# Performance work log

Hardware: AMD Instinct MI355X
Metric: run time of the kernel (lower is better)

The kernel has to match this reference:

```python
import jax, jax.numpy as jnp
import numpy as np

B, C, H, W = 2, 128, 64, 64
D_STATE, D_CONV, EXPAND = 16, 4, 2
D_INNER = EXPAND * C
DT_RANK = (C + 15) // 16  # ceil(d_model/16) = 8


def layernorm(x, w, b):
    # WithBias_LayerNorm over last (channel) dim, unbiased=False variance
    mu = jnp.mean(x, axis=-1, keepdims=True)
    var = jnp.mean((x - mu) ** 2, axis=-1, keepdims=True)
    return (x - mu) / jnp.sqrt(var + 1e-5) * w + b


def causal_conv1d_silu(x, w, b):
    # x: (b, d, l); w: (d, k) depthwise; causal pad k-1 on left, then SiLU
    k = w.shape[1]
    out = jax.lax.conv_general_dilated(
        x, w[:, None, :], window_strides=(1,), padding=[(k - 1, 0)],
        dimension_numbers=('NCH', 'OIH', 'NCH'), feature_group_count=w.shape[0])
    return jax.nn.silu(out + b[:, None])


def selective_scan(dA, dBu, Cm):
    # dA, dBu: (b, d, l, n); Cm: (b, n, l) -> y: (b, d, l)
    dA_t = jnp.moveaxis(dA, 2, 0)    # (l, b, d, n)
    dBu_t = jnp.moveaxis(dBu, 2, 0)  # (l, b, d, n)
    C_t = jnp.moveaxis(Cm, 2, 0)     # (l, b, n)

    def step(h, inp):
        a, bu, c = inp
        h = a * h + bu
        y = jnp.einsum('bdn,bn->bd', h, c)
        return h, y

    h0 = jnp.zeros(dA.shape[:2] + (dA.shape[3],), dA.dtype)
    _, ys = jax.lax.scan(step, h0, (dA_t, dBu_t, C_t))
    return jnp.moveaxis(ys, 0, 2)  # (b, d, l)


def mamba_branch(x3, W_in, W_z, conv_w, conv_b, W_x, W_dt, b_dt, A, D, W_out):
    # x3: (b, l, d_model) normalized input
    x = jnp.einsum('bld,ed->bel', x3, W_in)  # (b, d_inner, l)
    z = jnp.einsum('bld,ed->bel', x3, W_z)
    x = causal_conv1d_silu(x, conv_w, conv_b)
    xdbl = jnp.einsum('bdl,ed->bel', x, W_x)  # (b, dt_rank+2n, l)
    dt_low = xdbl[:, :DT_RANK]
    Bm = xdbl[:, DT_RANK:DT_RANK + D_STATE]
    Cm = xdbl[:, DT_RANK + D_STATE:]
    delta = jax.nn.softplus(jnp.einsum('brl,dr->bdl', dt_low, W_dt) + b_dt[:, None])
    dA = jnp.exp(delta[:, :, :, None] * A[None, :, None, :])           # (b,d,l,n)
    dBu = jnp.einsum('bdl,bnl->bdln', delta * x, Bm)                    # (b,d,l,n)
    y = selective_scan(dA, dBu, Cm)
    y = y + D[:, None] * x
    y = y * jax.nn.silu(z)
    return jnp.einsum('bdl,od->blo', y, W_out)  # (b, l, d_model)


def setup_inputs() -> dict:
    key = jax.random.key(0)
    ks = jax.random.split(key, 24)
    rn = lambda k, shp, s: jax.random.normal(k, shp, dtype=jnp.float32) * s
    inp = {}
    inp['pan'] = rn(ks[0], (B, C, H, W), 1.0)
    inp['ms'] = rn(ks[1], (B, C, H, W), 1.0)
    inp['norm_w_pan'] = jnp.ones((C,), jnp.float32)
    inp['norm_b_pan'] = jnp.zeros((C,), jnp.float32)
    inp['norm_w_ms'] = jnp.ones((C,), jnp.float32)
    inp['norm_b_ms'] = jnp.zeros((C,), jnp.float32)
    inp['W_in_pan'] = rn(ks[2], (D_INNER, C), C ** -0.5)
    inp['W_in_ms'] = rn(ks[3], (D_INNER, C), C ** -0.5)
    inp['W_z_pan'] = rn(ks[4], (D_INNER, C), C ** -0.5)
    inp['W_z_ms'] = rn(ks[5], (D_INNER, C), C ** -0.5)
    inp['conv_w_pan'] = rn(ks[6], (D_INNER, D_CONV), D_CONV ** -0.5)
    inp['conv_b_pan'] = rn(ks[7], (D_INNER,), 0.02)
    inp['conv_w_ms'] = rn(ks[8], (D_INNER, D_CONV), D_CONV ** -0.5)
    inp['conv_b_ms'] = rn(ks[9], (D_INNER,), 0.02)
    inp['W_x_pan'] = rn(ks[10], (DT_RANK + 2 * D_STATE, D_INNER), D_INNER ** -0.5)
    inp['W_x_ms'] = rn(ks[11], (DT_RANK + 2 * D_STATE, D_INNER), D_INNER ** -0.5)
    dt_std = DT_RANK ** -0.5
    inp['W_dt_pan'] = jax.random.uniform(ks[12], (D_INNER, DT_RANK), jnp.float32, -dt_std, dt_std)
    inp['W_dt_ms'] = jax.random.uniform(ks[13], (D_INNER, DT_RANK), jnp.float32, -dt_std, dt_std)
    # dt bias init: inverse-softplus of dt ~ logU[1e-3, 1e-1]
    u = np.asarray(jax.random.uniform(ks[14], (D_INNER,)))
    dt = np.exp(u * (np.log(0.1) - np.log(0.001)) + np.log(0.001)).clip(min=1e-4)
    inv_dt = dt + np.log(-np.expm1(-dt))
    inp['b_dt_pan'] = jnp.asarray(inv_dt, jnp.float32)
    inp['b_dt_ms'] = jnp.asarray(inv_dt, jnp.float32)
    inp['A_log'] = jnp.log(jnp.broadcast_to(jnp.arange(1, D_STATE + 1, dtype=jnp.float32), (D_INNER, D_STATE)))
    inp['D_pan'] = jnp.ones((D_INNER,), jnp.float32)
    inp['D_ms'] = jnp.ones((D_INNER,), jnp.float32)
    inp['W_out_pan'] = rn(ks[15], (C, D_INNER), D_INNER ** -0.5)
    inp['W_out_ms'] = rn(ks[16], (C, D_INNER), D_INNER ** -0.5)
    return inp


def reference(pan, ms, norm_w_pan, norm_b_pan, norm_w_ms, norm_b_ms,
              W_in_pan, W_in_ms, W_z_pan, W_z_ms,
              conv_w_pan, conv_b_pan, conv_w_ms, conv_b_ms,
              W_x_pan, W_x_ms, W_dt_pan, W_dt_ms, b_dt_pan, b_dt_ms,
              A_log, D_pan, D_ms, W_out_pan, W_out_ms):
    b, c, h, w = pan.shape
    A = -jnp.exp(A_log)
    pan3 = layernorm(pan.reshape(b, c, h * w).transpose(0, 2, 1), norm_w_pan, norm_b_pan)
    ms3 = layernorm(ms.reshape(b, c, h * w).transpose(0, 2, 1), norm_w_ms, norm_b_ms)
    out_pan = mamba_branch(pan3, W_in_pan, W_z_pan, conv_w_pan, conv_b_pan,
                           W_x_pan, W_dt_pan, b_dt_pan, A, D_pan, W_out_pan)
    out_ms = mamba_branch(ms3, W_in_ms, W_z_ms, conv_w_ms, conv_b_ms,
                          W_x_ms, W_dt_ms, b_dt_ms, A, D_ms, W_out_ms)
    out_pan = out_pan.transpose(0, 2, 1).reshape(b, c, h, w)
    out_ms = out_ms.transpose(0, 2, 1).reshape(b, c, h, w)
    return (out_pan, out_ms)
```

## Files before the change

### kernel.cpp

```cpp
#include <hip/hip_runtime.h>
#include <hip/hip_bf16.h>

constexpr int BB = 2;
constexpr int CC = 128;
constexpr int LL = 4096;
constexpr int DI = 256;
constexpr int DS = 16;
constexpr int DR = 8;
constexpr int DX = 40;
constexpr int NZ = 2 * BB;
constexpr int CH = 8;
constexpr int NCH = LL / CH;
constexpr int SEG = 32;

typedef short bf16x8 __attribute__((ext_vector_type(8)));
typedef float f32x4 __attribute__((ext_vector_type(4)));
typedef float f32x2 __attribute__((ext_vector_type(2)));

__device__ __forceinline__ unsigned short f2bf(float x) {
    __hip_bfloat16 h = __float2bfloat16(x);
    return *(unsigned short*)&h;
}
__device__ __forceinline__ float bflo(unsigned u) { return __uint_as_float(u << 16); }
__device__ __forceinline__ float bfhi(unsigned u) { return __uint_as_float(u & 0xffff0000u); }
__device__ __forceinline__ float bfu(unsigned short u) { return __uint_as_float((unsigned)u << 16); }
__device__ __forceinline__ float fast_rcp(float x) { return __builtin_amdgcn_rcpf(x); }
__device__ __forceinline__ float siluf(float x) { return x * fast_rcp(1.f + __expf(-x)); }
__device__ __forceinline__ float softplusf(float x) {
    const float z = exp2f(x * 1.44269504f);
    return (x > 20.f) ? x : 0.69314718f * log2f(1.f + z);
}
__device__ __forceinline__ unsigned pk2(float lo, float hi) {
    return (unsigned)f2bf(lo) | ((unsigned)f2bf(hi) << 16);
}
__device__ __forceinline__ bf16x8 cvt8(const float4 a, const float4 b) {
    bf16x8 r;
    r[0] = (short)f2bf(a.x); r[1] = (short)f2bf(a.y);
    r[2] = (short)f2bf(a.z); r[3] = (short)f2bf(a.w);
    r[4] = (short)f2bf(b.x); r[5] = (short)f2bf(b.y);
    r[6] = (short)f2bf(b.z); r[7] = (short)f2bf(b.w);
    return r;
}

__global__ __launch_bounds__(256) void gemm_inz_mfma(
    const float* __restrict__ pan, const float* __restrict__ ms,
    const float* __restrict__ wpan, const float* __restrict__ bpan,
    const float* __restrict__ wms, const float* __restrict__ bms,
    const float* __restrict__ Winp, const float* __restrict__ Winm,
    const float* __restrict__ Wzp, const float* __restrict__ Wzm,
    unsigned short* __restrict__ xpre16, unsigned short* __restrict__ zb16)
{
    const int zi = blockIdx.z;
    const int my = blockIdx.y;
    const bool br = (zi >= BB);
    const float* WIf = br ? Winm : Winp;
    const float* WZf = br ? Wzm : Wzp;
    const float* inp = br ? ms : pan;
    const float* wln = br ? wms : wpan;
    const float* bln = br ? bms : bpan;
    const int mbase = my * 64;
    const int n0 = blockIdx.x * 64;
    const int t = threadIdx.x;
    const int w = t >> 6, ln = t & 63;
    const int nf = ln & 15, qb = ln >> 4;
    const int kp = t >> 4, n4 = (t & 15) * 4;

    bf16x8 afragI[4], afragZ[4];
    const int mrow = mbase + w * 16 + nf;
    #pragma unroll
    for (int c = 0; c < 4; c++) {
        const float* pi = WIf + (size_t)mrow * CC + c * 32 + qb * 8;
        const float* pz = WZf + (size_t)mrow * CC + c * 32 + qb * 8;
        afragI[c] = cvt8(*(const float4*)pi, *(const float4*)(pi + 4));
        afragZ[c] = cvt8(*(const float4*)pz, *(const float4*)(pz + 4));
    }

    const float* xbase = inp + (size_t)(zi & 1) * CC * LL + n0 + n4;
    float xv[8][4];
    float wrow[8], brow[8];
    float sm[4] = {}, sq[4] = {};
    #pragma unroll
    for (int j = 0; j < 8; j++) {
        const int r = (j >> 1) * 32 + 2 * kp + (j & 1);
        const float4 v = *(const float4*)(xbase + (size_t)r * LL);
        xv[j][0] = v.x; xv[j][1] = v.y; xv[j][2] = v.z; xv[j][3] = v.w;
        wrow[j] = wln[r]; brow[j] = bln[r];
        sm[0] += v.x; sm[1] += v.y; sm[2] += v.z; sm[3] += v.w;
        sq[0] += v.x * v.x; sq[1] += v.y * v.y; sq[2] += v.z * v.z; sq[3] += v.w * v.w;
    }
    __shared__ float redS[16][64];
    __shared__ float redQ[16][64];
    #pragma unroll
    for (int j = 0; j < 4; j++) { redS[kp][n4 + j] = sm[j]; redQ[kp][n4 + j] = sq[j]; }
    __syncthreads();
    float mu[4], rs[4];
    #pragma unroll
    for (int j = 0; j < 4; j++) { sm[j] = 0.f; sq[j] = 0.f; }
    #pragma unroll
    for (int k = 0; k < 16; k++)
        #pragma unroll
        for (int j = 0; j < 4; j++) { sm[j] += redS[k][n4 + j]; sq[j] += redQ[k][n4 + j]; }
    #pragma unroll
    for (int j = 0; j < 4; j++) {
        mu[j] = sm[j] * (1.f / CC);
        rs[j] = rsqrtf(sq[j] * (1.f / CC) - mu[j] * mu[j] + 1e-5f);
    }
    unsigned pk[4][4];
    #pragma unroll
    for (int kc = 0; kc < 4; kc++)
        #pragma unroll
        for (int j = 0; j < 4; j++) {
            const float lo = (xv[kc * 2 + 0][j] - mu[j]) * rs[j] * wrow[kc * 2 + 0] + brow[kc * 2 + 0];
            const float hi = (xv[kc * 2 + 1][j] - mu[j]) * rs[j] * wrow[kc * 2 + 1] + brow[kc * 2 + 1];
            pk[kc][j] = pk2(lo, hi);
        }

    __shared__ unsigned short Bs[64][40];
    unsigned* Bw = (unsigned*)Bs;
    f32x4 accI[4] = {}, accZ[4] = {};
    #pragma unroll
    for (int kc = 0; kc < 4; kc++) {
        if (kc) __syncthreads();
        Bw[(n4 + 0) * 20 + kp] = pk[kc][0];
        Bw[(n4 + 1) * 20 + kp] = pk[kc][1];
        Bw[(n4 + 2) * 20 + kp] = pk[kc][2];
        Bw[(n4 + 3) * 20 + kp] = pk[kc][3];
        __syncthreads();
        #pragma unroll
        for (int ns = 0; ns < 4; ns++) {
            const bf16x8 bf = *(const bf16x8*)(&Bs[ns * 16 + nf][qb * 8]);
            accI[ns] = __builtin_amdgcn_mfma_f32_16x16x32_bf16(afragI[kc], bf, accI[ns], 0, 0, 0);
            accZ[ns] = __builtin_amdgcn_mfma_f32_16x16x32_bf16(afragZ[kc], bf, accZ[ns], 0, 0, 0);
        }
    }
    #pragma unroll
    for (int ns = 0; ns < 4; ns++)
        #pragma unroll
        for (int r = 0; r < 4; r++) {
            const int m = mbase + w * 16 + qb * 4 + r;
            xpre16[((size_t)zi * DI + m) * LL + n0 + ns * 16 + nf] = f2bf(accI[ns][r]);
            zb16  [((size_t)zi * DI + m) * LL + n0 + ns * 16 + nf] = f2bf(siluf(accZ[ns][r]));
        }
}

__global__ __launch_bounds__(256) void gemm_x_mfma(
    const float* __restrict__ Wxp, const float* __restrict__ Wxm,
    const unsigned short* __restrict__ xpre16,
    const float* __restrict__ cw0, const float* __restrict__ cb0,
    const float* __restrict__ cw1, const float* __restrict__ cb1,
    unsigned short* __restrict__ xc, unsigned short* __restrict__ xdbl16)
{
    const int zi = blockIdx.z;
    const float* Wf = (zi >= BB) ? Wxm : Wxp;
    const float* cw = (zi >= BB) ? cw1 : cw0;
    const float* cb = (zi >= BB) ? cb1 : cb0;
    const unsigned short* Xb = xpre16 + (size_t)zi * DI * LL;
    unsigned short* xcb = xc + (size_t)zi * DI * LL;
    const int n0 = blockIdx.x * 64;
    const int t = threadIdx.x;
    const int w = t >> 6, ln = t & 63;
    const int nf = ln & 15, qb = ln >> 4;
    bf16x8 zfrag;
    #pragma unroll
    for (int j = 0; j < 8; j++) zfrag[j] = 0;
    bf16x8 afrag[8];
    const int mrow = w * 16 + nf;
    #pragma unroll
    for (int c = 0; c < 8; c++) {
        if (mrow < DX) {
            const float* p = Wf + (size_t)mrow * DI + c * 32 + qb * 8;
            afrag[c] = cvt8(*(const float4*)p, *(const float4*)(p + 4));
        } else afrag[c] = zfrag;
    }
    __shared__ unsigned short Bs[64][40];
    unsigned* Bw = (unsigned*)Bs;
    f32x4 acc[4] = {};
    const int kp = t >> 4, n4 = (t & 15) * 4;
    const bool edge = (n0 + n4 == 0);
    ushort4 cur0, cur1, prv0, prv1;
    {
        const unsigned short* xp0 = Xb + (size_t)(2 * kp) * LL + n0 + n4;
        const unsigned short* xp1 = Xb + (size_t)(2 * kp + 1) * LL + n0 + n4;
        cur0 = *(const ushort4*)xp0; cur1 = *(const ushort4*)xp1;
        if (!edge) { prv0 = *(const ushort4*)(xp0 - 4); prv1 = *(const ushort4*)(xp1 - 4); }
        else { prv0 = ushort4{0,0,0,0}; prv1 = ushort4{0,0,0,0}; }
    }
    #pragma unroll
    for (int kc = 0; kc < 8; kc++) {
        ushort4 o[2];
        #pragma unroll
        for (int rr = 0; rr < 2; rr++) {
            const int e = kc * 32 + 2 * kp + rr;
            const ushort4 cur = rr ? cur1 : cur0;
            const ushort4 prv = rr ? prv1 : prv0;
            const float xm3 = bfu(prv.y), xm2 = bfu(prv.z), xm1 = bfu(prv.w);
            const float c0 = bfu(cur.x), c1 = bfu(cur.y);
            const float c2 = bfu(cur.z), c3 = bfu(cur.w);
            const float w0 = cw[e * 4 + 0], w1 = cw[e * 4 + 1];
            const float w2 = cw[e * 4 + 2], w3 = cw[e * 4 + 3];
            const float bias = cb[e];
            o[rr].x = f2bf(siluf(w0 * xm3 + w1 * xm2 + w2 * xm1 + w3 * c0 + bias));
            o[rr].y = f2bf(siluf(w0 * xm2 + w1 * xm1 + w2 * c0 + w3 * c1 + bias));
            o[rr].z = f2bf(siluf(w0 * xm1 + w1 * c0 + w2 * c1 + w3 * c2 + bias));
            o[rr].w = f2bf(siluf(w0 * c0 + w1 * c1 + w2 * c2 + w3 * c3 + bias));
        }
        *(ushort4*)(xcb + (size_t)(kc * 32 + 2 * kp) * LL + n0 + n4) = o[0];
        *(ushort4*)(xcb + (size_t)(kc * 32 + 2 * kp + 1) * LL + n0 + n4) = o[1];
        if (kc) __syncthreads();
        Bw[(n4 + 0) * 20 + kp] = (unsigned)(unsigned short)o[0].x | ((unsigned)(unsigned short)o[1].x << 16);
        Bw[(n4 + 1) * 20 + kp] = (unsigned)(unsigned short)o[0].y | ((unsigned)(unsigned short)o[1].y << 16);
        Bw[(n4 + 2) * 20 + kp] = (unsigned)(unsigned short)o[0].z | ((unsigned)(unsigned short)o[1].z << 16);
        Bw[(n4 + 3) * 20 + kp] = (unsigned)(unsigned short)o[0].w | ((unsigned)(unsigned short)o[1].w << 16);
        __syncthreads();
        if (kc < 7) {
            const unsigned short* xp0 = Xb + (size_t)((kc + 1) * 32 + 2 * kp) * LL + n0 + n4;
            const unsigned short* xp1 = Xb + (size_t)((kc + 1) * 32 + 2 * kp + 1) * LL + n0 + n4;
            cur0 = *(const ushort4*)xp0; cur1 = *(const ushort4*)xp1;
            if (!edge) { prv0 = *(const ushort4*)(xp0 - 4); prv1 = *(const ushort4*)(xp1 - 4); }
        }
        #pragma unroll
        for (int ns = 0; ns < 4; ns++) {
            const bf16x8 bf = *(const bf16x8*)(&Bs[ns * 16 + nf][qb * 8]);
            acc[ns] = __builtin_amdgcn_mfma_f32_16x16x32_bf16(afrag[kc], bf, acc[ns], 0, 0, 0);
        }
    }
    #pragma unroll
    for (int ns = 0; ns < 4; ns++)
        #pragma unroll
        for (int r = 0; r < 4; r++) {
            const int m = w * 16 + qb * 4 + r;
            if (m < DX)
                xdbl16[((size_t)zi * DX + m) * LL + n0 + ns * 16 + nf] = f2bf(acc[ns][r]);
        }
}

__global__ __launch_bounds__(256) void gemm_out_mfma(
    const float* __restrict__ Woutp, const float* __restrict__ Woutm,
    const unsigned short* __restrict__ yb, float* __restrict__ outg)
{
    const int zi = blockIdx.z;
    const float* Wf = (zi >= BB) ? Woutm : Woutp;
    const int mbase = blockIdx.y * 64;
    const unsigned short* Xb = yb + (size_t)zi * DI * LL;
    const int n0 = blockIdx.x * 64;
    const int t = threadIdx.x;
    const int w = t >> 6, ln = t & 63;
    const int nf = ln & 15, qb = ln >> 4;
    bf16x8 afrag[8];
    const int mrow = mbase + w * 16 + nf;
    #pragma unroll
    for (int c = 0; c < 8; c++) {
        const float* p = Wf + (size_t)mrow * DI + c * 32 + qb * 8;
        afrag[c] = cvt8(*(const float4*)p, *(const float4*)(p + 4));
    }
    __shared__ unsigned short Bs[64][40];
    unsigned* Bw = (unsigned*)Bs;
    f32x4 acc[4] = {};
    const int kp = t >> 4, n4 = (t & 15) * 4;
    ushort4 a0 = *(const ushort4*)(Xb + (size_t)(2 * kp) * LL + n0 + n4);
    ushort4 a1 = *(const ushort4*)(Xb + (size_t)(2 * kp + 1) * LL + n0 + n4);
    #pragma unroll
    for (int kc = 0; kc < 8; kc++) {
        if (kc) __syncthreads();
        Bw[(n4 + 0) * 20 + kp] = (unsigned)a0.x | ((unsigned)a1.x << 16);
        Bw[(n4 + 1) * 20 + kp] = (unsigned)a0.y | ((unsigned)a1.y << 16);
        Bw[(n4 + 2) * 20 + kp] = (unsigned)a0.z | ((unsigned)a1.z << 16);
        Bw[(n4 + 3) * 20 + kp] = (unsigned)a0.w | ((unsigned)a1.w << 16);
        __syncthreads();
        if (kc < 7) {
            a0 = *(const ushort4*)(Xb + (size_t)((kc + 1) * 32 + 2 * kp) * LL + n0 + n4);
            a1 = *(const ushort4*)(Xb + (size_t)((kc + 1) * 32 + 2 * kp + 1) * LL + n0 + n4);
        }
        #pragma unroll
        for (int ns = 0; ns < 4; ns++) {
            const bf16x8 bf = *(const bf16x8*)(&Bs[ns * 16 + nf][qb * 8]);
            acc[ns] = __builtin_amdgcn_mfma_f32_16x16x32_bf16(afrag[kc], bf, acc[ns], 0, 0, 0);
        }
    }
    #pragma unroll
    for (int ns = 0; ns < 4; ns++)
        #pragma unroll
        for (int r = 0; r < 4; r++) {
            const int m = mbase + w * 16 + qb * 4 + r;
            outg[((size_t)zi * CC + m) * LL + n0 + ns * 16 + nf] = acc[ns][r];
        }
}

__global__ __launch_bounds__(512, 8) void scan_fused(
    const unsigned short* __restrict__ xc, const unsigned short* __restrict__ xdbl16,
    const float* __restrict__ A_log,
    const float* __restrict__ Wdt0, const float* __restrict__ Wdt1,
    const float* __restrict__ bdt0, const float* __restrict__ bdt1,
    const float* __restrict__ D0, const float* __restrict__ D1,
    const unsigned short* __restrict__ zb16, unsigned short* __restrict__ yb)
{
    const int blk = blockIdx.x;
    const int zi = blk >> 8;
    const int d  = blk & (DI - 1);
    const int t = threadIdx.x;
    const int l0 = t * CH;
    __shared__ float Ssh[DS * (NCH + 1)];
    __shared__ float sdl_sh[NCH];
    __shared__ float Pseg[DS * (SEG + 1)];
    __shared__ float Sseg[DS * (SEG + 1)];
    const unsigned short* xdb = xdbl16 + (size_t)zi * DX * LL;
    const float* Wdt = (zi >= BB) ? Wdt1 : Wdt0;
    const float* bdt = (zi >= BB) ? bdt1 : bdt0;
    const float dbias = bdt[d];
    float rx[CH];
    {
        const uint4 xv4 = *(const uint4*)(xc + (size_t)blk * LL + l0);
        rx[0] = bflo(xv4.x); rx[1] = bfhi(xv4.x);
        rx[2] = bflo(xv4.y); rx[3] = bfhi(xv4.y);
        rx[4] = bflo(xv4.z); rx[5] = bfhi(xv4.z);
        rx[6] = bflo(xv4.w); rx[7] = bfhi(xv4.w);
    }
    float e[CH], rdlx[CH];
    {
        f32x2 acc2[4];
        #pragma unroll
        for (int j = 0; j < 4; j++) acc2[j] = f32x2{dbias, dbias};
        #pragma unroll
        for (int r = 0; r < DR; r++) {
            const float wr = Wdt[d * DR + r];
            const f32x2 w2 = {wr, wr};
            const uint4 v = *(const uint4*)(xdb + (size_t)r * LL + l0);
            acc2[0] = w2 * f32x2{bflo(v.x), bfhi(v.x)} + acc2[0];
            acc2[1] = w2 * f32x2{bflo(v.y), bfhi(v.y)} + acc2[1];
            acc2[2] = w2 * f32x2{bflo(v.z), bfhi(v.z)} + acc2[2];
            acc2[3] = w2 * f32x2{bflo(v.w), bfhi(v.w)} + acc2[3];
        }
        float av[CH];
        av[0] = acc2[0].x; av[1] = acc2[0].y; av[2] = acc2[1].x; av[3] = acc2[1].y;
        av[4] = acc2[2].x; av[5] = acc2[2].y; av[6] = acc2[3].x; av[7] = acc2[3].y;
        float sdl = 0.f;
        #pragma unroll
        for (int i = 0; i < CH; i++) {
            const float sp = softplusf(av[i]);
            sdl += sp;
            rdlx[i] = sp * rx[i];
            e[i] = __expf(-sp);
        }
        sdl_sh[t] = sdl;
    }
    bool fast = true;
    #pragma unroll
    for (int n = 0; n < DS; n++)
        fast = fast && (fabsf(__expf(A_log[d * DS + n]) - (float)(n + 1)) < 1e-3f);
    const unsigned short* Bbase = xdb + (size_t)DR * LL;
    const unsigned short* Cbase = Bbase + (size_t)DS * LL;
    float y[CH];
    const int n2 = t & 15, sg = t >> 4;

    if (fast) {
        f32x2 e2[4], rdlx2[4];
        #pragma unroll
        for (int j = 0; j < 4; j++) {
            e2[j] = f32x2{e[2 * j], e[2 * j + 1]};
            rdlx2[j] = f32x2{rdlx[2 * j], rdlx[2 * j + 1]};
        }
        f32x2 pw2[4];
        #pragma unroll
        for (int j = 0; j < 4; j++) pw2[j] = f32x2{1.f, 1.f};
        #pragma unroll 4
        for (int n = 0; n < DS; n++) {
            const uint4 bv = *(const uint4*)(Bbase + (size_t)n * LL + l0);
            const f32x2 b0 = {bflo(bv.x), bfhi(bv.x)};
            const f32x2 b1 = {bflo(bv.y), bfhi(bv.y)};
            const f32x2 b2 = {bflo(bv.z), bfhi(bv.z)};
            const f32x2 b3 = {bflo(bv.w), bfhi(bv.w)};
            pw2[0] *= e2[0]; pw2[1] *= e2[1]; pw2[2] *= e2[2]; pw2[3] *= e2[3];
            const f32x2 u0 = rdlx2[0] * b0, u1 = rdlx2[1] * b1;
            const f32x2 u2 = rdlx2[2] * b2, u3 = rdlx2[3] * b3;
            float hn = u0.x;
            hn = fmaf(pw2[0].y, hn, u0.y);
            hn = fmaf(pw2[1].x, hn, u1.x);
            hn = fmaf(pw2[1].y, hn, u1.y);
            hn = fmaf(pw2[2].x, hn, u2.x);
            hn = fmaf(pw2[2].y, hn, u2.y);
            hn = fmaf(pw2[3].x, hn, u3.x);
            hn = fmaf(pw2[3].y, hn, u3.y);
            Ssh[n * (NCH + 1) + t] = hn;
        }
        __syncthreads();
        float pcache[16];
        {
            const float Ann = -(float)(n2 + 1);
            float P = 1.f, S = 0.f;
            #pragma unroll
            for (int k = 0; k < 16; k++) {
                const int c = sg * 16 + k;
                const float p = __expf(Ann * sdl_sh[c]);
                pcache[k] = p;
                const float s = Ssh[n2 * (NCH + 1) + c];
                S = fmaf(p, S, s);
                P *= p;
            }
            Pseg[n2 * (SEG + 1) + sg] = P;
            Sseg[n2 * (SEG + 1) + sg] = S;
        }
        __syncthreads();
        if (t < DS) {
            float h = 0.f;
            #pragma unroll 4
            for (int c2 = 0; c2 < SEG; c2++) {
                const float p = Pseg[t * (SEG + 1) + c2];
                const float s = Sseg[t * (SEG + 1) + c2];
                Sseg[t * (SEG + 1) + c2] = h;
                h = fmaf(p, h, s);
            }
        }
        __syncthreads();
        {
            float h = Sseg[n2 * (SEG + 1) + sg];
            #pragma unroll
            for (int k = 0; k < 16; k++) {
                const int c = sg * 16 + k;
                const float s = Ssh[n2 * (NCH + 1) + c];
                Ssh[n2 * (NCH + 1) + c] = h;
                h = fmaf(pcache[k], h, s);
            }
        }
        __syncthreads();
        f32x2 y2[4];
        #pragma unroll
        for (int j = 0; j < 4; j++) { y2[j] = f32x2{0.f, 0.f}; pw2[j] = f32x2{1.f, 1.f}; }
        #pragma unroll 4
        for (int n = 0; n < DS; n++) {
            const uint4 bv = *(const uint4*)(Bbase + (size_t)n * LL + l0);
            const uint4 cv = *(const uint4*)(Cbase + (size_t)n * LL + l0);
            const f32x2 b0 = {bflo(bv.x), bfhi(bv.x)};
            const f32x2 b1 = {bflo(bv.y), bfhi(bv.y)};
            const f32x2 b2 = {bflo(bv.z), bfhi(bv.z)};
            const f32x2 b3 = {bflo(bv.w), bfhi(bv.w)};
            const f32x2 c0 = {bflo(cv.x), bfhi(cv.x)};
            const f32x2 c1 = {bflo(cv.y), bfhi(cv.y)};
            const f32x2 c2 = {bflo(cv.z), bfhi(cv.z)};
            const f32x2 c3 = {bflo(cv.w), bfhi(cv.w)};
            pw2[0] *= e2[0]; pw2[1] *= e2[1]; pw2[2] *= e2[2]; pw2[3] *= e2[3];
            const f32x2 u0 = rdlx2[0] * b0, u1 = rdlx2[1] * b1;
            const f32x2 u2 = rdlx2[2] * b2, u3 = rdlx2[3] * b3;
            const float hp = Ssh[n * (NCH + 1) + t];
            const float h0 = fmaf(pw2[0].x, hp, u0.x);
            const float h1 = fmaf(pw2[0].y, h0, u0.y);
            y2[0] = f32x2{h0, h1} * c0 + y2[0];
            const float h2 = fmaf(pw2[1].x, h1, u1.x);
            const float h3 = fmaf(pw2[1].y, h2, u1.y);
            y2[1] = f32x2{h2, h3} * c1 + y2[1];
            const float h4 = fmaf(pw2[2].x, h3, u2.x);
            const float h5 = fmaf(pw2[2].y, h4, u2.y);
            y2[2] = f32x2{h4, h5} * c2 + y2[2];
            const float h6 = fmaf(pw2[3].x, h5, u3.x);
            const float h7 = fmaf(pw2[3].y, h6, u3.y);
            y2[3] = f32x2{h6, h7} * c3 + y2[3];
        }
        y[0] = y2[0].x; y[1] = y2[0].y; y[2] = y2[1].x; y[3] = y2[1].y;
        y[4] = y2[2].x; y[5] = y2[2].y; y[6] = y2[3].x; y[7] = y2[3].y;
    } else {
        float rdl[CH];
        #pragma unroll
        for (int i = 0; i < CH; i++) rdl[i] = -0.69314718f * log2f(e[i]);
        #pragma unroll 2
        for (int n = 0; n < DS; n++) {
            const float An = -__expf(A_log[d * DS + n]);
            const uint4 bv = *(const uint4*)(Bbase + (size_t)n * LL + l0);
            float hn = 0.f;
            hn = fmaf(__expf(rdl[0] * An), hn, rdlx[0] * bflo(bv.x));
            hn = fmaf(__expf(rdl[1] * An), hn, rdlx[1] * bfhi(bv.x));
            hn = fmaf(__expf(rdl[2] * An), hn, rdlx[2] * bflo(bv.y));
            hn = fmaf(__expf(rdl[3] * An), hn, rdlx[3] * bfhi(bv.y));
            hn = fmaf(__expf(rdl[4] * An), hn, rdlx[4] * bflo(bv.z));
            hn = fmaf(__expf(rdl[5] * An), hn, rdlx[5] * bfhi(bv.z));
            hn = fmaf(__expf(rdl[6] * An), hn, rdlx[6] * bflo(bv.w));
            hn = fmaf(__expf(rdl[7] * An), hn, rdlx[7] * bfhi(bv.w));
            Ssh[n * (NCH + 1) + t] = hn;
        }
        __syncthreads();
        {
            const float Ann = -__expf(A_log[d * DS + n2]);
            float P = 1.f, S = 0.f;
            #pragma unroll
            for (int k = 0; k < 16; k++) {
                const int c = sg * 16 + k;
                const float p = __expf(Ann * sdl_sh[c]);
                const float s = Ssh[n2 * (NCH + 1) + c];
                S = fmaf(p, S, s);
                P *= p;
            }
            Pseg[n2 * (SEG + 1) + sg] = P;
            Sseg[n2 * (SEG + 1) + sg] = S;
        }
        __syncthreads();
        if (t < DS) {
            float h = 0.f;
            #pragma unroll 4
            for (int c2 = 0; c2 < SEG; c2++) {
                const float p = Pseg[t * (SEG + 1) + c2];
                const float s = Sseg[t * (SEG + 1) + c2];
                Sseg[t * (SEG + 1) + c2] = h;
                h = fmaf(p, h, s);
            }
        }
        __syncthreads();
        {
            const float Ann = -__expf(A_log[d * DS + n2]);
            float h = Sseg[n2 * (SEG + 1) + sg];
            #pragma unroll
            for (int k = 0; k < 16; k++) {
                const int c = sg * 16 + k;
                const float p = __expf(Ann * sdl_sh[c]);
                const float s = Ssh[n2 * (NCH + 1) + c];
                Ssh[n2 * (NCH + 1) + c] = h;
                h = fmaf(p, h, s);
            }
        }
        __syncthreads();
        #pragma unroll
        for (int i = 0; i < CH; i++) y[i] = 0.f;
        #pragma unroll 2
        for (int n = 0; n < DS; n++) {
            const float An = -__expf(A_log[d * DS + n]);
            const uint4 bv = *(const uint4*)(Bbase + (size_t)n * LL + l0);
            const uint4 cv = *(const uint4*)(Cbase + (size_t)n * LL + l0);
            float hn = Ssh[n * (NCH + 1) + t];
            hn = fmaf(__expf(rdl[0] * An), hn, rdlx[0] * bflo(bv.x)); y[0] = fmaf(hn, bflo(cv.x), y[0]);
            hn = fmaf(__expf(rdl[1] * An), hn, rdlx[1] * bfhi(bv.x)); y[1] = fmaf(hn, bfhi(cv.x), y[1]);
            hn = fmaf(__expf(rdl[2] * An), hn, rdlx[2] * bflo(bv.y)); y[2] = fmaf(hn, bflo(cv.y), y[2]);
            hn = fmaf(__expf(rdl[3] * An), hn, rdlx[3] * bfhi(bv.y)); y[3] = fmaf(hn, bfhi(cv.y), y[3]);
            hn = fmaf(__expf(rdl[4] * An), hn, rdlx[4] * bflo(bv.z)); y[4] = fmaf(hn, bflo(cv.z), y[4]);
            hn = fmaf(__expf(rdl[5] * An), hn, rdlx[5] * bfhi(bv.z)); y[5] = fmaf(hn, bfhi(cv.z), y[5]);
            hn = fmaf(__expf(rdl[6] * An), hn, rdlx[6] * bflo(bv.w)); y[6] = fmaf(hn, bflo(cv.w), y[6]);
            hn = fmaf(__expf(rdl[7] * An), hn, rdlx[7] * bfhi(bv.w)); y[7] = fmaf(hn, bfhi(cv.w), y[7]);
        }
    }
    const float Dd = ((zi >= BB) ? D1 : D0)[d];
    const unsigned short* z_g = zb16 + (size_t)blk * LL + l0;
    unsigned short* y_g = yb + (size_t)blk * LL + l0;
    {
        const uint4 zv = *(const uint4*)z_g;
        float zf[CH];
        zf[0] = bflo(zv.x); zf[1] = bfhi(zv.x); zf[2] = bflo(zv.y); zf[3] = bfhi(zv.y);
        zf[4] = bflo(zv.z); zf[5] = bfhi(zv.z); zf[6] = bflo(zv.w); zf[7] = bfhi(zv.w);
        ushort4 r0, r1;
        #pragma unroll
        for (int i = 0; i < CH; i++) {
            const float val = (y[i] + Dd * rx[i]) * zf[i];
            if (i < 4) ((unsigned short*)&r0)[i] = f2bf(val);
            else       ((unsigned short*)&r1)[i - 4] = f2bf(val);
        }
        *(ushort4*)(y_g + 0) = r0;
        *(ushort4*)(y_g + 4) = r1;
    }
}

extern "C" void kernel_launch(void* const* d_in, const int* in_sizes, int n_in,
                              void* d_out, int out_size, void* d_ws, size_t ws_size,
                              hipStream_t stream)
{
    (void)in_sizes; (void)n_in; (void)out_size; (void)ws_size;
    auto fp = [&](int i) { return (const float*)d_in[i]; };
    const float *pan = fp(0), *ms = fp(1);
    const float *nwp = fp(2), *nbp = fp(3), *nwm = fp(4), *nbm = fp(5);
    const float *Winp = fp(6), *Winm = fp(7), *Wzp = fp(8), *Wzm = fp(9);
    const float *cwp = fp(10), *cbp = fp(11), *cwm = fp(12), *cbm = fp(13);
    const float *Wxp = fp(14), *Wxm = fp(15);
    const float *Wdtp = fp(16), *Wdtm = fp(17), *bdtp = fp(18), *bdtm = fp(19);
    const float *Alog = fp(20), *Dp = fp(21), *Dm = fp(22);
    const float *Woutp = fp(23), *Woutm = fp(24);

    unsigned short* us = (unsigned short*)d_ws;
    unsigned short* xpre16 = us;
    unsigned short* zb16   = xpre16 + (size_t)NZ * DI * LL;
    unsigned short* xdbl16 = zb16   + (size_t)NZ * DI * LL;
    unsigned short* yb     = xdbl16 + (size_t)NZ * DX * LL;
    unsigned short* xc     = yb     + (size_t)NZ * DI * LL;
    float* out = (float*)d_out;

    gemm_inz_mfma<<<dim3(LL / 64, 4, NZ), 256, 0, stream>>>(
        pan, ms, nwp, nbp, nwm, nbm, Winp, Winm, Wzp, Wzm, xpre16, zb16);
    gemm_x_mfma<<<dim3(LL / 64, 1, NZ), 256, 0, stream>>>(
        Wxp, Wxm, xpre16, cwp, cbp, cwm, cbm, xc, xdbl16);
    scan_fused<<<dim3(NZ * DI), 512, 0, stream>>>(xc, xdbl16, Alog, Wdtp, Wdtm, bdtp, bdtm,
                                                  Dp, Dm, zb16, yb);
    gemm_out_mfma<<<dim3(LL / 64, 2, NZ), 256, 0, stream>>>(Woutp, Woutm, yb, out);
}
```

Before: 178.2 us.

## Split layernorm into its own kernel producing bf16 normalized activations

```diff
diff --git a/kernel.cpp b/kernel.cpp
--- a/kernel.cpp
+++ b/kernel.cpp
@@ -30,9 +30,6 @@
     const float z = exp2f(x * 1.44269504f);
     return (x > 20.f) ? x : 0.69314718f * log2f(1.f + z);
 }
-__device__ __forceinline__ unsigned pk2(float lo, float hi) {
-    return (unsigned)f2bf(lo) | ((unsigned)f2bf(hi) << 16);
-}
 __device__ __forceinline__ bf16x8 cvt8(const float4 a, const float4 b) {
     bf16x8 r;
     r[0] = (short)f2bf(a.x); r[1] = (short)f2bf(a.y);
@@ -42,12 +39,49 @@
     return r;
 }
 
-__global__ __launch_bounds__(256) void gemm_inz_mfma(
+__global__ __launch_bounds__(256) void layernorm_kernel(
     const float* __restrict__ pan, const float* __restrict__ ms,
     const float* __restrict__ wpan, const float* __restrict__ bpan,
     const float* __restrict__ wms, const float* __restrict__ bms,
+    unsigned short* __restrict__ x3b)
+{
+    const int zi = blockIdx.y;
+    const int br = zi >> 1, b = zi & 1;
+    const float* inp = br ? ms : pan;
+    const float* wp = br ? wms : wpan;
+    const float* bp = br ? bms : bpan;
+    const int l0 = blockIdx.x * 64;
+    const int t = threadIdx.x;
+    const int lo = t & 63, c4 = t >> 6;
+    const float* base = inp + (size_t)b * CC * LL + l0 + lo;
+    float vals[32];
+    float s = 0.f, s2 = 0.f;
+    #pragma unroll
+    for (int i = 0; i < 32; i++) {
+        const int c = c4 * 32 + i;
+        const float v = base[(size_t)c * LL];
+        vals[i] = v; s += v; s2 += v * v;
+    }
+    __shared__ float red[2][4][64];
+    red[0][c4][lo] = s; red[1][c4][lo] = s2;
+    __syncthreads();
+    const float S  = red[0][0][lo] + red[0][1][lo] + red[0][2][lo] + red[0][3][lo];
+    const float S2 = red[1][0][lo] + red[1][1][lo] + red[1][2][lo] + red[1][3][lo];
+    const float mu = S * (1.f / CC);
+    const float var = S2 * (1.f / CC) - mu * mu;
+    const float rstd = rsqrtf(var + 1e-5f);
+    unsigned short* out = x3b + (size_t)zi * CC * LL + l0 + lo;
+    #pragma unroll
+    for (int i = 0; i < 32; i++) {
+        const int c = c4 * 32 + i;
+        out[(size_t)c * LL] = f2bf((vals[i] - mu) * rstd * wp[c] + bp[c]);
+    }
+}
+
+__global__ __launch_bounds__(256) void gemm_inz_mfma(
     const float* __restrict__ Winp, const float* __restrict__ Winm,
     const float* __restrict__ Wzp, const float* __restrict__ Wzm,
+    const unsigned short* __restrict__ x3b,
     unsigned short* __restrict__ xpre16, unsigned short* __restrict__ zb16)
 {
     const int zi = blockIdx.z;
@@ -55,16 +89,12 @@
     const bool br = (zi >= BB);
     const float* WIf = br ? Winm : Winp;
     const float* WZf = br ? Wzm : Wzp;
-    const float* inp = br ? ms : pan;
-    const float* wln = br ? wms : wpan;
-    const float* bln = br ? bms : bpan;
     const int mbase = my * 64;
+    const unsigned short* Xb = x3b + (size_t)zi * CC * LL;
     const int n0 = blockIdx.x * 64;
     const int t = threadIdx.x;
     const int w = t >> 6, ln = t & 63;
     const int nf = ln & 15, qb = ln >> 4;
-    const int kp = t >> 4, n4 = (t & 15) * 4;
-
     bf16x8 afragI[4], afragZ[4];
     const int mrow = mbase + w * 16 + nf;
     #pragma unroll
@@ -74,58 +104,24 @@
         afragI[c] = cvt8(*(const float4*)pi, *(const float4*)(pi + 4));
         afragZ[c] = cvt8(*(const float4*)pz, *(const float4*)(pz + 4));
     }
-
-    const float* xbase = inp + (size_t)(zi & 1) * CC * LL + n0 + n4;
-    float xv[8][4];
-    float wrow[8], brow[8];
-    float sm[4] = {}, sq[4] = {};
-    #pragma unroll
-    for (int j = 0; j < 8; j++) {
-        const int r = (j >> 1) * 32 + 2 * kp + (j & 1);
-        const float4 v = *(const float4*)(xbase + (size_t)r * LL);
-        xv[j][0] = v.x; xv[j][1] = v.y; xv[j][2] = v.z; xv[j][3] = v.w;
-        wrow[j] = wln[r]; brow[j] = bln[r];
-        sm[0] += v.x; sm[1] += v.y; sm[2] += v.z; sm[3] += v.w;
-        sq[0] += v.x * v.x; sq[1] += v.y * v.y; sq[2] += v.z * v.z; sq[3] += v.w * v.w;
-    }
-    __shared__ float redS[16][64];
-    __shared__ float redQ[16][64];
-    #pragma unroll
-    for (int j = 0; j < 4; j++) { redS[kp][n4 + j] = sm[j]; redQ[kp][n4 + j] = sq[j]; }
-    __syncthreads();
-    float mu[4], rs[4];
-    #pragma unroll
-    for (int j = 0; j < 4; j++) { sm[j] = 0.f; sq[j] = 0.f; }
-    #pragma unroll
-    for (int k = 0; k < 16; k++)
-        #pragma unroll
-        for (int j = 0; j < 4; j++) { sm[j] += redS[k][n4 + j]; sq[j] += redQ[k][n4 + j]; }
-    #pragma unroll
-    for (int j = 0; j < 4; j++) {
-        mu[j] = sm[j] * (1.f / CC);
-        rs[j] = rsqrtf(sq[j] * (1.f / CC) - mu[j] * mu[j] + 1e-5f);
-    }
-    unsigned pk[4][4];
-    #pragma unroll
-    for (int kc = 0; kc < 4; kc++)
-        #pragma unroll
-        for (int j = 0; j < 4; j++) {
-            const float lo = (xv[kc * 2 + 0][j] - mu[j]) * rs[j] * wrow[kc * 2 + 0] + brow[kc * 2 + 0];
-            const float hi = (xv[kc * 2 + 1][j] - mu[j]) * rs[j] * wrow[kc * 2 + 1] + brow[kc * 2 + 1];
-            pk[kc][j] = pk2(lo, hi);
-        }
-
     __shared__ unsigned short Bs[64][40];
     unsigned* Bw = (unsigned*)Bs;
     f32x4 accI[4] = {}, accZ[4] = {};
+    const int kp = t >> 4, n4 = (t & 15) * 4;
+    ushort4 a0 = *(const ushort4*)(Xb + (size_t)(2 * kp) * LL + n0 + n4);
+    ushort4 a1 = *(const ushort4*)(Xb + (size_t)(2 * kp + 1) * LL + n0 + n4);
     #pragma unroll
     for (int kc = 0; kc < 4; kc++) {
         if (kc) __syncthreads();
-        Bw[(n4 + 0) * 20 + kp] = pk[kc][0];
-        Bw[(n4 + 1) * 20 + kp] = pk[kc][1];
-        Bw[(n4 + 2) * 20 + kp] = pk[kc][2];
-        Bw[(n4 + 3) * 20 + kp] = pk[kc][3];
-        __syncthreads();
+        Bw[(n4 + 0) * 20 + kp] = (unsigned)a0.x | ((unsigned)a1.x << 16);
+        Bw[(n4 + 1) * 20 + kp] = (unsigned)a0.y | ((unsigned)a1.y << 16);
+        Bw[(n4 + 2) * 20 + kp] = (unsigned)a0.z | ((unsigned)a1.z << 16);
+        Bw[(n4 + 3) * 20 + kp] = (unsigned)a0.w | ((unsigned)a1.w << 16);
+        __syncthreads();
+        if (kc < 3) {
+            a0 = *(const ushort4*)(Xb + (size_t)((kc + 1) * 32 + 2 * kp) * LL + n0 + n4);
+            a1 = *(const ushort4*)(Xb + (size_t)((kc + 1) * 32 + 2 * kp + 1) * LL + n0 + n4);
+        }
         #pragma unroll
         for (int ns = 0; ns < 4; ns++) {
             const bf16x8 bf = *(const bf16x8*)(&Bs[ns * 16 + nf][qb * 8]);
@@ -569,15 +565,18 @@
     const float *Woutp = fp(23), *Woutm = fp(24);
 
     unsigned short* us = (unsigned short*)d_ws;
-    unsigned short* xpre16 = us;
+    unsigned short* x3b    = us;
+    unsigned short* xpre16 = x3b    + (size_t)NZ * CC * LL;
     unsigned short* zb16   = xpre16 + (size_t)NZ * DI * LL;
     unsigned short* xdbl16 = zb16   + (size_t)NZ * DI * LL;
     unsigned short* yb     = xdbl16 + (size_t)NZ * DX * LL;
     unsigned short* xc     = yb     + (size_t)NZ * DI * LL;
     float* out = (float*)d_out;
 
+    layernorm_kernel<<<dim3(LL / 64, NZ), 256, 0, stream>>>(
+        pan, ms, nwp, nbp, nwm, nbm, x3b);
     gemm_inz_mfma<<<dim3(LL / 64, 4, NZ), 256, 0, stream>>>(
-        pan, ms, nwp, nbp, nwm, nbm, Winp, Winm, Wzp, Wzm, xpre16, zb16);
+        Winp, Winm, Wzp, Wzm, x3b, xpre16, zb16);
     gemm_x_mfma<<<dim3(LL / 64, 1, NZ), 256, 0, stream>>>(
         Wxp, Wxm, xpre16, cwp, cbp, cwm, cbm, xc, xdbl16);
     scan_fused<<<dim3(NZ * DI), 512, 0, stream>>>(xc, xdbl16, Alog, Wdtp, Wdtm, bdtp, bdtm,
```

New measurement: 175.9 us. Within noise of the previous version (-1.3%).
